# Optimization experiments

Measured on AMD Instinct MI355X. Metric: run time of the kernel, lower is better.

Reference implementation:

```python
import jax, jax.numpy as jnp
import numpy as np

MODEL_DIM = 1024
H = 16
DK = MODEL_DIM // H


def setup_inputs() -> dict:
    key = jax.random.key(0)
    ks = jax.random.split(key, 11)
    B, S, D = 4, 2048, MODEL_DIM
    s = 1.0 / np.sqrt(D)
    inp = {
        "q": jax.random.normal(ks[0], (B, S, D), jnp.float32),
        "k": jax.random.normal(ks[1], (B, S, D), jnp.float32),
        "v": jax.random.normal(ks[2], (B, S, D), jnp.float32),
        # stacked per-head projection weights [H, D, DK] and biases [H, DK]
        "wq_w": jax.random.normal(ks[3], (H, D, DK), jnp.float32) * s,
        "wq_b": jax.random.normal(ks[4], (H, DK), jnp.float32) * s,
        "wk_w": jax.random.normal(ks[5], (H, D, DK), jnp.float32) * s,
        "wk_b": jax.random.normal(ks[6], (H, DK), jnp.float32) * s,
        "wv_w": jax.random.normal(ks[7], (H, D, DK), jnp.float32) * s,
        "wv_b": jax.random.normal(ks[8], (H, DK), jnp.float32) * s,
        "wo_w": jax.random.normal(ks[9], (D, D), jnp.float32) * s,
        "wo_b": jax.random.normal(ks[10], (D,), jnp.float32) * s,
    }
    return inp


def reference(q, k, v, wq_w, wq_b, wk_w, wk_b, wv_w, wv_b, wo_w, wo_b):
    # per-head projections, batched over heads: [B,S,D] x [H,D,DK] -> [B,H,S,DK]
    qh = jnp.einsum('bsd,hdk->bhsk', q, wq_w) + wq_b[None, :, None, :]
    kh = jnp.einsum('bsd,hdk->bhsk', k, wk_w) + wk_b[None, :, None, :]
    vh = jnp.einsum('bsd,hdk->bhsk', v, wv_w) + wv_b[None, :, None, :]
    scale = 1.0 / jnp.sqrt(jnp.asarray(DK, qh.dtype))
    scores = jnp.einsum('bhqk,bhsk->bhqs', qh, kh) * scale  # [B,H,S,S]
    out = jnp.einsum('bhqs,bhsk->bhqk', scores, vh)         # [B,H,S,DK]
    # NON-STANDARD: softmax applied AFTER the value matmul, over last dim (dv)
    out = jax.nn.softmax(out, axis=-1)
    # concat heads along feature dim: [B,S,H*DK]
    B, Hh, S, Dk = out.shape
    heads = jnp.transpose(out, (0, 2, 1, 3)).reshape(B, S, Hh * Dk)
    return heads @ wo_w.T + wo_b
```

## Files before the change

### kernel.cpp

```cpp
#include <hip/hip_runtime.h>
#include <math.h>

#define B 4
#define S 2048
#define D 1024
#define H 16
#define DK 64
#define MS (B * S)
#define GKA 2048

typedef short bf16x8 __attribute__((ext_vector_type(8)));
typedef float f32x4 __attribute__((ext_vector_type(4)));

__device__ __forceinline__ unsigned short f2bf(float x) {
  union { float f; unsigned u; } v; v.f = x;
  unsigned r = v.u + 0x7fff + ((v.u >> 16) & 1);
  return (unsigned short)(r >> 16);
}
__device__ __forceinline__ float bf2f(unsigned short h) {
  union { unsigned u; float f; } v; v.u = ((unsigned)h) << 16;
  return v.f;
}
__device__ __forceinline__ void split2(float x, unsigned short& hi, unsigned short& lo) {
  hi = f2bf(x);
  lo = f2bf(x - bf2f(hi));
}

__global__ __launch_bounds__(256) void prep_kernel(
    const float* __restrict__ q, const float* __restrict__ k, const float* __restrict__ v,
    const float* __restrict__ wk, const float* __restrict__ wv, const float* __restrict__ wq,
    const float* __restrict__ wo,
    unsigned short* __restrict__ KSP, unsigned short* __restrict__ VSP,
    unsigned short* __restrict__ QSP,
    unsigned short* __restrict__ WKS, unsigned short* __restrict__ WVS,
    unsigned short* __restrict__ WQA, unsigned short* __restrict__ WOB,
    float* __restrict__ M) {
  const int blk = blockIdx.x;
  const int tid = threadIdx.x;
  if (blk < 24576) {
    const int which = blk >> 13;
    const int bb = blk & 8191;
    const float* X = which == 0 ? k : (which == 1 ? v : q);
    unsigned short* O = which == 0 ? KSP : (which == 1 ? VSP : QSP);
    int t = bb * 256 + tid;
    int idx = t * 4;
    int m = idx >> 10, d = idx & 1023;
    float4 x = *(const float4*)&X[idx];
    union { unsigned short h[4]; ushort4 u; } uh, ul;
    split2(x.x, uh.h[0], ul.h[0]);
    split2(x.y, uh.h[1], ul.h[1]);
    split2(x.z, uh.h[2], ul.h[2]);
    split2(x.w, uh.h[3], ul.h[3]);
    *(ushort4*)&O[(size_t)m * GKA + d] = uh.u;
    *(ushort4*)&O[(size_t)m * GKA + 1024 + d] = ul.u;
  } else if (blk < 32768) {
    const int which = (blk - 24576) >> 12;
    const int bb = (blk - 24576) & 4095;
    const float* W = which == 0 ? wk : wv;
    unsigned short* O = which == 0 ? WKS : WVS;
    int t = bb * 256 + tid;
    int d = t & 1023, n = t >> 10;
    int h = n >> 6, dk = n & 63;
    float x = W[((size_t)(h << 10) + d) * 64 + dk];
    unsigned short hi, lo;
    split2(x, hi, lo);
    size_t ro = (size_t)n * GKA + d;
    O[ro] = hi;
    O[ro + 1024] = lo;
  } else if (blk < 36864) {
    int t = (blk - 32768) * 256 + tid;
    int kk = t & 63;
    int hd = t >> 6;
    float x = wq[t];
    unsigned short hi, lo;
    split2(x, hi, lo);
    WQA[(size_t)hd * 128 + kk] = hi;
    WQA[(size_t)hd * 128 + 64 + kk] = lo;
  } else if (blk < 37888) {
    int t = (blk - 36864) * 256 + tid;
    int idx = t * 4;
    float4 x = *(const float4*)&wo[idx];
    ushort4 u;
    u.x = f2bf(x.x); u.y = f2bf(x.y); u.z = f2bf(x.z); u.w = f2bf(x.w);
    *(ushort4*)&WOB[idx] = u;
  } else {
    int t = (blk - 37888) * 256 + tid;
    *(float4*)&M[(size_t)t * 4] = (float4){0.f, 0.f, 0.f, 0.f};
  }
}

__device__ __forceinline__ void gll(const unsigned short* g, unsigned short* l) {
  __builtin_amdgcn_global_load_lds((const __attribute__((address_space(1))) void*)g,
                                   (__attribute__((address_space(3))) void*)l, 16, 0, 0);
}

template <int NWC>
__device__ __forceinline__ void stageT(
    const unsigned short* __restrict__ A, const unsigned short* __restrict__ BT,
    const unsigned* aoffs, const unsigned* boffs,
    unsigned short* Asb, unsigned short* Bsb, int aof, int bof, int w) {
#pragma unroll
  for (int g = 0; g < 4; ++g) gll(A + aoffs[g] + aof, Asb + g * 4096 + w * 512);
#pragma unroll
  for (int g = 0; g < NWC; ++g) gll(BT + boffs[g] + bof, Bsb + g * 4096 + w * 512);
}

template <int NWC, int EPI, int KLOG>
__global__ __launch_bounds__(512, 2) void gemm256(
    const unsigned short* __restrict__ A0, const unsigned short* __restrict__ A1,
    const unsigned short* __restrict__ Bt0, const unsigned short* __restrict__ Bt1,
    const float* __restrict__ bias0, const float* __restrict__ bias1,
    void* __restrict__ C0, void* __restrict__ C1) {
  constexpr int NWR = 8 / NWC;
  constexpr int MR = (256 / NWR) / 16;
  constexpr int NPH = MR / 2;
  constexpr int BN = NWC * 64;
  constexpr int AST = (KLOG == 1024) ? 1024 : 2048;
  constexpr int NKT = KLOG / 64;
  constexpr int GX = 1024 / BN;
  constexpr int NWG = GX * 32;
  constexpr int CPX = NWG / 8;

  __shared__ __align__(16) unsigned short As[2][256 * 64];
  __shared__ __align__(16) unsigned short Bs[2][BN * 64];

  const int tid = threadIdx.x;
  const int lane = tid & 63;
  const int w = tid >> 6;
  const int wr = w / NWC;
  const int wc = w % NWC;
  const int fm = lane & 15;
  const int quad = lane >> 4;
  const int sx = (fm & 7) << 3;

  int lin = blockIdx.y * GX + blockIdx.x;
  lin = (lin & 7) * CPX + (lin >> 3);
  const int bxs = lin & (GX - 1);
  const int bys = lin / GX;
  const size_t bm = (size_t)bys * 256;
  const size_t bn = (size_t)bxs * BN;

  const unsigned short* A;
  const unsigned short* BT;
  const float* bias;
  if constexpr (EPI == 1) {
    const int b = bys >> 3;
    A = A0;
    BT = Bt0 + (size_t)b * D * GKA;
    bias = bias0 + (size_t)b * D;
  } else {
    A = blockIdx.z ? A1 : A0;
    BT = blockIdx.z ? Bt1 : Bt0;
    bias = blockIdx.z ? bias1 : bias0;
  }

  const int srow = tid >> 3;
  const int scol = ((tid & 7) ^ (srow & 7)) << 3;
  unsigned aoffs[4], boffs[NWC];
#pragma unroll
  for (int g = 0; g < 4; ++g) aoffs[g] = (unsigned)((bm + g * 64 + srow) * AST + scol);
#pragma unroll
  for (int g = 0; g < NWC; ++g) boffs[g] = (unsigned)((bn + g * 64 + srow) * AST + scol);

  const int basek0 = (quad * 8) ^ sx;
  const int basek1 = (32 + quad * 8) ^ sx;
  const int arow0 = (wr * (MR * 16) + fm) * 64;
  const int brow0 = (wc * 64 + fm) * 64;

  f32x4 acc[MR][4];
#pragma unroll
  for (int i = 0; i < MR; ++i)
#pragma unroll
    for (int j = 0; j < 4; ++j) acc[i][j] = (f32x4){0.f, 0.f, 0.f, 0.f};

  auto ka = [](int k0) { return (KLOG == 3072) ? (k0 < 2048 ? k0 : k0 - 2048) : k0; };
  auto kb = [](int k0) { return (KLOG == 3072) ? (k0 < 1024 ? k0 : k0 - 1024) : k0; };

  stageT<NWC>(A, BT, aoffs, boffs, As[0], Bs[0], ka(0), kb(0), w);
  stageT<NWC>(A, BT, aoffs, boffs, As[1], Bs[1], ka(64), kb(64), w);

#pragma unroll 1
  for (int t = 0; t < NKT; ++t) {
    const unsigned short* Ab = As[t & 1];
    const unsigned short* Bb = Bs[t & 1];
    unsigned short* Asb = As[t & 1];
    unsigned short* Bsb = Bs[t & 1];

    if (t < NKT - 1) {
      if constexpr (NWC == 4) asm volatile("s_waitcnt vmcnt(8)" ::: "memory");
      else                    asm volatile("s_waitcnt vmcnt(6)" ::: "memory");
    } else {
      asm volatile("s_waitcnt vmcnt(0)" ::: "memory");
    }
    __builtin_amdgcn_s_barrier();
    __builtin_amdgcn_sched_barrier(0);

    bf16x8 bfr[4][2];
    bf16x8 afr[2][2][2];

#pragma unroll
    for (int j = 0; j < 4; ++j) {
      bfr[j][0] = *(const bf16x8*)&Bb[brow0 + j * 1024 + basek0];
      bfr[j][1] = *(const bf16x8*)&Bb[brow0 + j * 1024 + basek1];
    }
#pragma unroll
    for (int ii = 0; ii < 2; ++ii) {
      afr[0][ii][0] = *(const bf16x8*)&Ab[arow0 + ii * 1024 + basek0];
      afr[0][ii][1] = *(const bf16x8*)&Ab[arow0 + ii * 1024 + basek1];
    }
    __builtin_amdgcn_sched_barrier(0);

#pragma unroll
    for (int qq = 0; qq < NPH; ++qq) {
      if (qq + 1 < NPH) {
#pragma unroll
        for (int ii = 0; ii < 2; ++ii) {
          afr[(qq + 1) & 1][ii][0] =
              *(const bf16x8*)&Ab[arow0 + ((qq + 1) * 2 + ii) * 1024 + basek0];
          afr[(qq + 1) & 1][ii][1] =
              *(const bf16x8*)&Ab[arow0 + ((qq + 1) * 2 + ii) * 1024 + basek1];
        }
        asm volatile("s_waitcnt lgkmcnt(4)" ::: "memory");
      } else {
        asm volatile("s_waitcnt lgkmcnt(0)" ::: "memory");
      }
      __builtin_amdgcn_sched_barrier(0);
      __builtin_amdgcn_s_setprio(1);
#pragma unroll
      for (int ii = 0; ii < 2; ++ii)
#pragma unroll
        for (int j = 0; j < 4; ++j) {
          acc[qq * 2 + ii][j] = __builtin_amdgcn_mfma_f32_16x16x32_bf16(
              afr[qq & 1][ii][0], bfr[j][0], acc[qq * 2 + ii][j], 0, 0, 0);
          acc[qq * 2 + ii][j] = __builtin_amdgcn_mfma_f32_16x16x32_bf16(
              afr[qq & 1][ii][1], bfr[j][1], acc[qq * 2 + ii][j], 0, 0, 0);
        }
      __builtin_amdgcn_s_setprio(0);
      __builtin_amdgcn_sched_barrier(0);
    }

    __builtin_amdgcn_s_barrier();
    if (t + 2 < NKT) {
      const int k0 = (t + 2) * 64;
      stageT<NWC>(A, BT, aoffs, boffs, Asb, Bsb, ka(k0), kb(k0), w);
    }
  }

  if constexpr (EPI == 0) {
    float* C = (float*)(blockIdx.z ? C1 : C0);
#pragma unroll
    for (int i = 0; i < MR; ++i)
#pragma unroll
      for (int j = 0; j < 4; ++j) {
        size_t row = bm + wr * (MR * 16) + i * 16 + quad * 4;
        size_t col = bn + wc * 64 + j * 16 + fm;
        float bb = bias[col];
#pragma unroll
        for (int r = 0; r < 4; ++r) C[(row + r) * D + col] = acc[i][j][r] + bb;
      }
  } else {
    unsigned short* HB = (unsigned short*)C0;
    const size_t head_col0 = bn + wc * 64;
    float bj[4];
#pragma unroll
    for (int j = 0; j < 4; ++j) bj[j] = bias[head_col0 + j * 16 + fm];
#pragma unroll
    for (int i = 0; i < MR; ++i) {
      f32x4 val[4];
#pragma unroll
      for (int j = 0; j < 4; ++j)
#pragma unroll
        for (int r = 0; r < 4; ++r) val[j][r] = (acc[i][j][r] + bj[j]) * 0.125f;

      f32x4 mx = val[0];
#pragma unroll
      for (int j = 1; j < 4; ++j)
#pragma unroll
        for (int r = 0; r < 4; ++r) mx[r] = fmaxf(mx[r], val[j][r]);
#pragma unroll
      for (int off = 1; off < 16; off <<= 1)
#pragma unroll
        for (int r = 0; r < 4; ++r) mx[r] = fmaxf(mx[r], __shfl_xor(mx[r], off, 64));

      f32x4 e[4];
      f32x4 sm = (f32x4){0.f, 0.f, 0.f, 0.f};
#pragma unroll
      for (int j = 0; j < 4; ++j)
#pragma unroll
        for (int r = 0; r < 4; ++r) {
          e[j][r] = __expf(val[j][r] - mx[r]);
          sm[r] += e[j][r];
        }
#pragma unroll
      for (int off = 1; off < 16; off <<= 1)
#pragma unroll
        for (int r = 0; r < 4; ++r) sm[r] += __shfl_xor(sm[r], off, 64);

      f32x4 inv;
#pragma unroll
      for (int r = 0; r < 4; ++r) inv[r] = 1.0f / sm[r];

#pragma unroll
      for (int j = 0; j < 4; ++j)
#pragma unroll
        for (int r = 0; r < 4; ++r) {
          size_t row = bm + wr * (MR * 16) + i * 16 + quad * 4 + r;
          HB[row * D + head_col0 + j * 16 + fm] = f2bf(e[j][r] * inv[r]);
        }
    }
  }
}

__global__ __launch_bounds__(256) void compute_m_kernel(
    const float* __restrict__ KH, const float* __restrict__ VH, float* __restrict__ Mout) {
  const int sc = blockIdx.x, h = blockIdx.y, b = blockIdx.z;
  const int tid = threadIdx.x;
  const int i0 = (tid >> 4) * 4;
  const int j0 = (tid & 15) * 4;
  __shared__ float ks[16][64], vs[16][64];
  float acc[4][4];
#pragma unroll
  for (int a = 0; a < 4; a++)
#pragma unroll
    for (int c = 0; c < 4; c++) acc[a][c] = 0.f;

  const int s0 = sc * (S / 8);
  const int rr = tid >> 4;
  const int cc = (tid & 15) * 4;
  for (int s = s0; s < s0 + S / 8; s += 16) {
    size_t base = ((size_t)b * S + s + rr) * D + h * 64 + cc;
    __syncthreads();
    *(float4*)&ks[rr][cc] = *(const float4*)&KH[base];
    *(float4*)&vs[rr][cc] = *(const float4*)&VH[base];
    __syncthreads();
#pragma unroll
    for (int ss = 0; ss < 16; ss++) {
      float4 kf = *(const float4*)&ks[ss][i0];
      float4 vf = *(const float4*)&vs[ss][j0];
      float ka[4] = {kf.x, kf.y, kf.z, kf.w};
      float va[4] = {vf.x, vf.y, vf.z, vf.w};
#pragma unroll
      for (int a = 0; a < 4; a++)
#pragma unroll
        for (int c = 0; c < 4; c++) acc[a][c] += ka[a] * va[c];
    }
  }
  float* Mp = Mout + ((size_t)(b * H + h)) * DK * DK;
#pragma unroll
  for (int a = 0; a < 4; a++)
#pragma unroll
    for (int c = 0; c < 4; c++) atomicAdd(&Mp[(i0 + a) * DK + j0 + c], acc[a][c]);
}

__global__ __launch_bounds__(256) void split_m_bias_kernel(
    const float* __restrict__ M, const float* __restrict__ bq,
    unsigned short* __restrict__ MSP, float* __restrict__ BQM) {
  const int bh = blockIdx.x;
  const int h = bh & 15;
  const float* Mp = M + (size_t)bh * 4096;
  unsigned short* hiP = MSP + (size_t)bh * 8192;
  unsigned short* loP = hiP + 4096;
  for (int idx = threadIdx.x; idx < 4096; idx += 256) {
    int kk = idx >> 6, nn = idx & 63;
    unsigned short hi, lo;
    split2(Mp[idx], hi, lo);
    hiP[nn * 64 + kk] = hi;
    loP[nn * 64 + kk] = lo;
  }
  if (threadIdx.x < 64) {
    int j = threadIdx.x;
    float a = 0.f;
#pragma unroll 8
    for (int kk = 0; kk < 64; kk++) a += bq[h * 64 + kk] * Mp[kk * 64 + j];
    BQM[(size_t)bh * 64 + j] = a;
  }
}

__global__ __launch_bounds__(256) void wqm_kernel(
    const unsigned short* __restrict__ WQA, const unsigned short* __restrict__ MSP,
    unsigned short* __restrict__ WQM) {
  const int c = blockIdx.x, h = blockIdx.y, b = blockIdx.z;
  const int tid = threadIdx.x;
  const int lane = tid & 63;
  const int w = tid >> 6;
  const int fm = lane & 15;
  const int quad = lane >> 4;
  const int ko = quad * 8;
  const int dbase = c * 64 + w * 16;

  const unsigned short* arow = WQA + ((size_t)h * 1024 + dbase + fm) * 128;
  bf16x8 ahi0 = *(const bf16x8*)&arow[ko];
  bf16x8 ahi1 = *(const bf16x8*)&arow[32 + ko];
  bf16x8 alo0 = *(const bf16x8*)&arow[64 + ko];
  bf16x8 alo1 = *(const bf16x8*)&arow[96 + ko];

  const unsigned short* hiP = MSP + ((size_t)(b * H + h)) * 8192;
  const unsigned short* loP = hiP + 4096;
  f32x4 acc[4];
#pragma unroll
  for (int j = 0; j < 4; j++) acc[j] = (f32x4){0.f, 0.f, 0.f, 0.f};
#pragma unroll
  for (int j = 0; j < 4; j++) {
    bf16x8 bhi0 = *(const bf16x8*)&hiP[(j * 16 + fm) * 64 + ko];
    bf16x8 bhi1 = *(const bf16x8*)&hiP[(j * 16 + fm) * 64 + 32 + ko];
    bf16x8 blo0 = *(const bf16x8*)&loP[(j * 16 + fm) * 64 + ko];
    bf16x8 blo1 = *(const bf16x8*)&loP[(j * 16 + fm) * 64 + 32 + ko];
    acc[j] = __builtin_amdgcn_mfma_f32_16x16x32_bf16(ahi0, bhi0, acc[j], 0, 0, 0);
    acc[j] = __builtin_amdgcn_mfma_f32_16x16x32_bf16(ahi1, bhi1, acc[j], 0, 0, 0);
    acc[j] = __builtin_amdgcn_mfma_f32_16x16x32_bf16(alo0, bhi0, acc[j], 0, 0, 0);
    acc[j] = __builtin_amdgcn_mfma_f32_16x16x32_bf16(alo1, bhi1, acc[j], 0, 0, 0);
    acc[j] = __builtin_amdgcn_mfma_f32_16x16x32_bf16(ahi0, blo0, acc[j], 0, 0, 0);
    acc[j] = __builtin_amdgcn_mfma_f32_16x16x32_bf16(ahi1, blo1, acc[j], 0, 0, 0);
  }

#pragma unroll
  for (int j = 0; j < 4; j++) {
    int n = h * 64 + j * 16 + fm;
    ushort4 hv, lv;
    unsigned short hi, lo;
    split2(acc[j][0], hi, lo); hv.x = hi; lv.x = lo;
    split2(acc[j][1], hi, lo); hv.y = hi; lv.y = lo;
    split2(acc[j][2], hi, lo); hv.z = hi; lv.z = lo;
    split2(acc[j][3], hi, lo); hv.w = hi; lv.w = lo;
    size_t base = ((size_t)b * D + n) * GKA + dbase + quad * 4;
    *(ushort4*)&WQM[base] = hv;
    *(ushort4*)&WQM[base + 1024] = lv;
  }
}

extern "C" void kernel_launch(void* const* d_in, const int* in_sizes, int n_in,
                              void* d_out, int out_size, void* d_ws, size_t ws_size,
                              hipStream_t stream) {
  const float* q = (const float*)d_in[0];
  const float* k = (const float*)d_in[1];
  const float* v = (const float*)d_in[2];
  const float* wq_w = (const float*)d_in[3];
  const float* wq_b = (const float*)d_in[4];
  const float* wk_w = (const float*)d_in[5];
  const float* wk_b = (const float*)d_in[6];
  const float* wv_w = (const float*)d_in[7];
  const float* wv_b = (const float*)d_in[8];
  const float* wo_w = (const float*)d_in[9];
  const float* wo_b = (const float*)d_in[10];
  float* out = (float*)d_out;

  unsigned short* KSP = (unsigned short*)d_ws;
  unsigned short* VSP = KSP + (size_t)16 * 1024 * 1024;
  unsigned short* QSP = VSP + (size_t)16 * 1024 * 1024;
  float* VH = (float*)(QSP + (size_t)16 * 1024 * 1024);
  float* M = VH + (size_t)MS * D;
  unsigned short* WKS = (unsigned short*)(M + 256 * 1024);
  unsigned short* WVS = WKS + (size_t)2 * 1024 * 1024;
  unsigned short* WQA = WVS + (size_t)2 * 1024 * 1024;
  unsigned short* WOB = WQA + (size_t)2 * 1024 * 1024;
  float* KH = out;
  unsigned short* HB = KSP;
  unsigned short* WQM = KSP + (size_t)8 * 1024 * 1024;
  unsigned short* MSP = VSP;
  float* BQM = (float*)(VSP + 512 * 1024);

  dim3 blk(256);

  prep_kernel<<<38144, blk, 0, stream>>>(q, k, v, wk_w, wv_w, wq_w, wo_w,
                                         KSP, VSP, QSP, WKS, WVS, WQA, WOB, M);
  gemm256<4, 0, 3072><<<dim3(4, 32, 2), dim3(512), 0, stream>>>(
      KSP, VSP, WKS, WVS, wk_b, wv_b, KH, VH);
  compute_m_kernel<<<dim3(8, H, B), blk, 0, stream>>>(KH, VH, M);
  split_m_bias_kernel<<<64, blk, 0, stream>>>(M, wq_b, MSP, BQM);
  wqm_kernel<<<dim3(16, H, B), blk, 0, stream>>>(WQA, MSP, WQM);
  gemm256<2, 1, 3072><<<dim3(8, 32, 1), dim3(512), 0, stream>>>(
      QSP, nullptr, WQM, nullptr, BQM, nullptr, HB, nullptr);
  gemm256<2, 0, 1024><<<dim3(8, 32, 1), dim3(512), 0, stream>>>(
      HB, HB, WOB, WOB, wo_b, wo_b, out, out);
}
```

Baseline: 429.5 us.

## Interleave hi/lo bf16 split within K tiles to cut loop iterations

Replaces the concatenated-K (3072) formulation of the split-bf16 GEMMs with a mode that loads hi and lo chunks side by side into each LDS tile and issues three MFMAs (hh, lh, hl) per fragment pair. This reduces the number of K iterations, barriers and LDS fragment reloads from 48 tiles to 32 while keeping the MFMA count the same. It changes the swizzle/offset mapping and adds register pressure from separate hi/lo fragments.

```diff
diff --git a/kernel.cpp b/kernel.cpp
--- a/kernel.cpp
+++ b/kernel.cpp
@@ -98,14 +98,14 @@
 __device__ __forceinline__ void stageT(
     const unsigned short* __restrict__ A, const unsigned short* __restrict__ BT,
     const unsigned* aoffs, const unsigned* boffs,
-    unsigned short* Asb, unsigned short* Bsb, int aof, int bof, int w) {
-#pragma unroll
-  for (int g = 0; g < 4; ++g) gll(A + aoffs[g] + aof, Asb + g * 4096 + w * 512);
-#pragma unroll
-  for (int g = 0; g < NWC; ++g) gll(BT + boffs[g] + bof, Bsb + g * 4096 + w * 512);
-}
-
-template <int NWC, int EPI, int KLOG>
+    unsigned short* Asb, unsigned short* Bsb, int k0, int w) {
+#pragma unroll
+  for (int g = 0; g < 4; ++g) gll(A + aoffs[g] + k0, Asb + g * 4096 + w * 512);
+#pragma unroll
+  for (int g = 0; g < NWC; ++g) gll(BT + boffs[g] + k0, Bsb + g * 4096 + w * 512);
+}
+
+template <int NWC, int EPI, int MODE>
 __global__ __launch_bounds__(512, 2) void gemm256(
     const unsigned short* __restrict__ A0, const unsigned short* __restrict__ A1,
     const unsigned short* __restrict__ Bt0, const unsigned short* __restrict__ Bt1,
@@ -115,8 +115,9 @@
   constexpr int MR = (256 / NWR) / 16;
   constexpr int NPH = MR / 2;
   constexpr int BN = NWC * 64;
-  constexpr int AST = (KLOG == 1024) ? 1024 : 2048;
-  constexpr int NKT = KLOG / 64;
+  constexpr int AST = MODE ? 2048 : 1024;
+  constexpr int NKT = MODE ? 32 : 16;
+  constexpr int KSTEP = MODE ? 32 : 64;
   constexpr int GX = 1024 / BN;
   constexpr int NWG = GX * 32;
   constexpr int CPX = NWG / 8;
@@ -131,7 +132,7 @@
   const int wc = w % NWC;
   const int fm = lane & 15;
   const int quad = lane >> 4;
-  const int sx = (fm & 7) << 3;
+  const int f7 = fm & 7;
 
   int lin = blockIdx.y * GX + blockIdx.x;
   lin = (lin & 7) * CPX + (lin >> 3);
@@ -155,17 +156,25 @@
   }
 
   const int srow = tid >> 3;
-  const int scol = ((tid & 7) ^ (srow & 7)) << 3;
+  int colb;
+  if constexpr (MODE) {
+    const int tq = (tid & 7) ^ (srow & 7);
+    colb = (tq >> 1) * 8 + (tq & 1) * 1024;
+  } else {
+    colb = ((tid & 7) ^ (srow & 7)) << 3;
+  }
   unsigned aoffs[4], boffs[NWC];
 #pragma unroll
-  for (int g = 0; g < 4; ++g) aoffs[g] = (unsigned)((bm + g * 64 + srow) * AST + scol);
-#pragma unroll
-  for (int g = 0; g < NWC; ++g) boffs[g] = (unsigned)((bn + g * 64 + srow) * AST + scol);
-
-  const int basek0 = (quad * 8) ^ sx;
-  const int basek1 = (32 + quad * 8) ^ sx;
+  for (int g = 0; g < 4; ++g) aoffs[g] = (unsigned)((bm + g * 64 + srow) * AST + colb);
+#pragma unroll
+  for (int g = 0; g < NWC; ++g) boffs[g] = (unsigned)((bn + g * 64 + srow) * AST + colb);
+
   const int arow0 = (wr * (MR * 16) + fm) * 64;
   const int brow0 = (wc * 64 + fm) * 64;
+  const int khi = ((quad * 2) ^ f7) * 8;
+  const int klo = ((quad * 2 + 1) ^ f7) * 8;
+  const int basek0 = (quad * 8) ^ (f7 << 3);
+  const int basek1 = (32 + quad * 8) ^ (f7 << 3);
 
   f32x4 acc[MR][4];
 #pragma unroll
@@ -173,11 +182,8 @@
 #pragma unroll
     for (int j = 0; j < 4; ++j) acc[i][j] = (f32x4){0.f, 0.f, 0.f, 0.f};
 
-  auto ka = [](int k0) { return (KLOG == 3072) ? (k0 < 2048 ? k0 : k0 - 2048) : k0; };
-  auto kb = [](int k0) { return (KLOG == 3072) ? (k0 < 1024 ? k0 : k0 - 1024) : k0; };
-
-  stageT<NWC>(A, BT, aoffs, boffs, As[0], Bs[0], ka(0), kb(0), w);
-  stageT<NWC>(A, BT, aoffs, boffs, As[1], Bs[1], ka(64), kb(64), w);
+  stageT<NWC>(A, BT, aoffs, boffs, As[0], Bs[0], 0, w);
+  stageT<NWC>(A, BT, aoffs, boffs, As[1], Bs[1], KSTEP, w);
 
 #pragma unroll 1
   for (int t = 0; t < NKT; ++t) {
@@ -195,54 +201,99 @@
     __builtin_amdgcn_s_barrier();
     __builtin_amdgcn_sched_barrier(0);
 
-    bf16x8 bfr[4][2];
-    bf16x8 afr[2][2][2];
-
-#pragma unroll
-    for (int j = 0; j < 4; ++j) {
-      bfr[j][0] = *(const bf16x8*)&Bb[brow0 + j * 1024 + basek0];
-      bfr[j][1] = *(const bf16x8*)&Bb[brow0 + j * 1024 + basek1];
-    }
-#pragma unroll
-    for (int ii = 0; ii < 2; ++ii) {
-      afr[0][ii][0] = *(const bf16x8*)&Ab[arow0 + ii * 1024 + basek0];
-      afr[0][ii][1] = *(const bf16x8*)&Ab[arow0 + ii * 1024 + basek1];
-    }
-    __builtin_amdgcn_sched_barrier(0);
-
-#pragma unroll
-    for (int qq = 0; qq < NPH; ++qq) {
-      if (qq + 1 < NPH) {
-#pragma unroll
-        for (int ii = 0; ii < 2; ++ii) {
-          afr[(qq + 1) & 1][ii][0] =
-              *(const bf16x8*)&Ab[arow0 + ((qq + 1) * 2 + ii) * 1024 + basek0];
-          afr[(qq + 1) & 1][ii][1] =
-              *(const bf16x8*)&Ab[arow0 + ((qq + 1) * 2 + ii) * 1024 + basek1];
+    if constexpr (MODE) {
+      bf16x8 bh[4], bl[4];
+      bf16x8 ah[2][2], al[2][2];
+#pragma unroll
+      for (int j = 0; j < 4; ++j) {
+        bh[j] = *(const bf16x8*)&Bb[brow0 + j * 1024 + khi];
+        bl[j] = *(const bf16x8*)&Bb[brow0 + j * 1024 + klo];
+      }
+#pragma unroll
+      for (int ii = 0; ii < 2; ++ii) {
+        ah[0][ii] = *(const bf16x8*)&Ab[arow0 + ii * 1024 + khi];
+        al[0][ii] = *(const bf16x8*)&Ab[arow0 + ii * 1024 + klo];
+      }
+      __builtin_amdgcn_sched_barrier(0);
+
+#pragma unroll
+      for (int qq = 0; qq < NPH; ++qq) {
+        if (qq + 1 < NPH) {
+#pragma unroll
+          for (int ii = 0; ii < 2; ++ii) {
+            ah[(qq + 1) & 1][ii] =
+                *(const bf16x8*)&Ab[arow0 + ((qq + 1) * 2 + ii) * 1024 + khi];
+            al[(qq + 1) & 1][ii] =
+                *(const bf16x8*)&Ab[arow0 + ((qq + 1) * 2 + ii) * 1024 + klo];
+          }
+          asm volatile("s_waitcnt lgkmcnt(4)" ::: "memory");
+        } else {
+          asm volatile("s_waitcnt lgkmcnt(0)" ::: "memory");
         }
-        asm volatile("s_waitcnt lgkmcnt(4)" ::: "memory");
-      } else {
-        asm volatile("s_waitcnt lgkmcnt(0)" ::: "memory");
+        __builtin_amdgcn_sched_barrier(0);
+        __builtin_amdgcn_s_setprio(1);
+#pragma unroll
+        for (int ii = 0; ii < 2; ++ii)
+#pragma unroll
+          for (int j = 0; j < 4; ++j) {
+            acc[qq * 2 + ii][j] = __builtin_amdgcn_mfma_f32_16x16x32_bf16(
+                ah[qq & 1][ii], bh[j], acc[qq * 2 + ii][j], 0, 0, 0);
+            acc[qq * 2 + ii][j] = __builtin_amdgcn_mfma_f32_16x16x32_bf16(
+                al[qq & 1][ii], bh[j], acc[qq * 2 + ii][j], 0, 0, 0);
+            acc[qq * 2 + ii][j] = __builtin_amdgcn_mfma_f32_16x16x32_bf16(
+                ah[qq & 1][ii], bl[j], acc[qq * 2 + ii][j], 0, 0, 0);
+          }
+        __builtin_amdgcn_s_setprio(0);
+        __builtin_amdgcn_sched_barrier(0);
+      }
+    } else {
+      bf16x8 bfr[4][2];
+      bf16x8 afr[2][2][2];
+#pragma unroll
+      for (int j = 0; j < 4; ++j) {
+        bfr[j][0] = *(const bf16x8*)&Bb[brow0 + j * 1024 + basek0];
+        bfr[j][1] = *(const bf16x8*)&Bb[brow0 + j * 1024 + basek1];
+      }
+#pragma unroll
+      for (int ii = 0; ii < 2; ++ii) {
+        afr[0][ii][0] = *(const bf16x8*)&Ab[arow0 + ii * 1024 + basek0];
+        afr[0][ii][1] = *(const bf16x8*)&Ab[arow0 + ii * 1024 + basek1];
       }
       __builtin_amdgcn_sched_barrier(0);
-      __builtin_amdgcn_s_setprio(1);
-#pragma unroll
-      for (int ii = 0; ii < 2; ++ii)
-#pragma unroll
-        for (int j = 0; j < 4; ++j) {
-          acc[qq * 2 + ii][j] = __builtin_amdgcn_mfma_f32_16x16x32_bf16(
-              afr[qq & 1][ii][0], bfr[j][0], acc[qq * 2 + ii][j], 0, 0, 0);
-          acc[qq * 2 + ii][j] = __builtin_amdgcn_mfma_f32_16x16x32_bf16(
-              afr[qq & 1][ii][1], bfr[j][1], acc[qq * 2 + ii][j], 0, 0, 0);
+
+#pragma unroll
+      for (int qq = 0; qq < NPH; ++qq) {
+        if (qq + 1 < NPH) {
+#pragma unroll
+          for (int ii = 0; ii < 2; ++ii) {
+            afr[(qq + 1) & 1][ii][0] =
+                *(const bf16x8*)&Ab[arow0 + ((qq + 1) * 2 + ii) * 1024 + basek0];
+            afr[(qq + 1) & 1][ii][1] =
+                *(const bf16x8*)&Ab[arow0 + ((qq + 1) * 2 + ii) * 1024 + basek1];
+          }
+          asm volatile("s_waitcnt lgkmcnt(4)" ::: "memory");
+        } else {
+          asm volatile("s_waitcnt lgkmcnt(0)" ::: "memory");
         }
-      __builtin_amdgcn_s_setprio(0);
-      __builtin_amdgcn_sched_barrier(0);
+        __builtin_amdgcn_sched_barrier(0);
+        __builtin_amdgcn_s_setprio(1);
+#pragma unroll
+        for (int ii = 0; ii < 2; ++ii)
+#pragma unroll
+          for (int j = 0; j < 4; ++j) {
+            acc[qq * 2 + ii][j] = __builtin_amdgcn_mfma_f32_16x16x32_bf16(
+                afr[qq & 1][ii][0], bfr[j][0], acc[qq * 2 + ii][j], 0, 0, 0);
+            acc[qq * 2 + ii][j] = __builtin_amdgcn_mfma_f32_16x16x32_bf16(
+                afr[qq & 1][ii][1], bfr[j][1], acc[qq * 2 + ii][j], 0, 0, 0);
+          }
+        __builtin_amdgcn_s_setprio(0);
+        __builtin_amdgcn_sched_barrier(0);
+      }
     }
 
     __builtin_amdgcn_s_barrier();
     if (t + 2 < NKT) {
-      const int k0 = (t + 2) * 64;
-      stageT<NWC>(A, BT, aoffs, boffs, Asb, Bsb, ka(k0), kb(k0), w);
+      stageT<NWC>(A, BT, aoffs, boffs, Asb, Bsb, (t + 2) * KSTEP, w);
     }
   }
 
@@ -463,13 +514,13 @@
 
   prep_kernel<<<38144, blk, 0, stream>>>(q, k, v, wk_w, wv_w, wq_w, wo_w,
                                          KSP, VSP, QSP, WKS, WVS, WQA, WOB, M);
-  gemm256<4, 0, 3072><<<dim3(4, 32, 2), dim3(512), 0, stream>>>(
+  gemm256<4, 0, 1><<<dim3(4, 32, 2), dim3(512), 0, stream>>>(
       KSP, VSP, WKS, WVS, wk_b, wv_b, KH, VH);
   compute_m_kernel<<<dim3(8, H, B), blk, 0, stream>>>(KH, VH, M);
   split_m_bias_kernel<<<64, blk, 0, stream>>>(M, wq_b, MSP, BQM);
   wqm_kernel<<<dim3(16, H, B), blk, 0, stream>>>(WQA, MSP, WQM);
-  gemm256<2, 1, 3072><<<dim3(8, 32, 1), dim3(512), 0, stream>>>(
+  gemm256<2, 1, 1><<<dim3(8, 32, 1), dim3(512), 0, stream>>>(
       QSP, nullptr, WQM, nullptr, BQM, nullptr, HB, nullptr);
-  gemm256<2, 0, 1024><<<dim3(8, 32, 1), dim3(512), 0, stream>>>(
+  gemm256<2, 0, 0><<<dim3(8, 32, 1), dim3(512), 0, stream>>>(
       HB, HB, WOB, WOB, wo_b, wo_b, out, out);
 }
```

New measurement: 415.3 us. 1.03x faster.
